# Optimization experiments

Hardware: AMD Instinct MI355X
Metric: run time of the kernel (lower is better)

The kernel has to match this reference:

```python
import jax, jax.numpy as jnp
import numpy as np

B, N, DIN, D, NH, NL = 4, 256, 4, 64, 4, 2
DH = D // NH
EPS = 1e-5
SLOPE = 0.01  # torch LeakyReLU default negative_slope


def setup_inputs() -> dict:
    key = jax.random.key(0)
    ks = jax.random.split(key, 16)
    def p(k, shape, s=0.05):
        return jax.random.normal(k, shape, jnp.float32) * s
    return {
        "feature": jax.random.normal(ks[0], (B, N, N, DIN), jnp.float32),
        "W1": p(ks[1], (DIN, D)), "b1": jnp.zeros((D,), jnp.float32),
        "mw": p(ks[2], (NH, D)), "mb": jnp.zeros((NH,), jnp.float32),
        "bn_gamma": jnp.ones((D,), jnp.float32), "bn_beta": jnp.zeros((D,), jnp.float32),
        "Wq": p(ks[3], (NL, D, D)), "bq": jnp.zeros((NL, D), jnp.float32),
        "Wk": p(ks[4], (NL, D, D)), "bk": jnp.zeros((NL, D), jnp.float32),
        "Wv": p(ks[5], (NL, D, D)), "bv": jnp.zeros((NL, D), jnp.float32),
        "Wo": p(ks[6], (NL, D, D)), "bo": jnp.zeros((NL, D), jnp.float32),
        "ln1_g": jnp.ones((NL, D), jnp.float32), "ln1_b": jnp.zeros((NL, D), jnp.float32),
        "Wff1": p(ks[7], (NL, D, 2 * D)), "bff1": jnp.zeros((NL, 2 * D), jnp.float32),
        "Wff2": p(ks[8], (NL, 2 * D, D)), "bff2": jnp.zeros((NL, D), jnp.float32),
        "ln2_g": jnp.ones((NL, D), jnp.float32), "ln2_b": jnp.zeros((NL, D), jnp.float32),
    }


def _leaky(x):
    return jnp.where(x >= 0, x, SLOPE * x)


def _layer_norm(x, g, b):
    m = x.mean(axis=-1, keepdims=True)
    v = x.var(axis=-1, keepdims=True)
    return g * (x - m) / jnp.sqrt(v + EPS) + b


def reference(feature, W1, b1, mw, mb, bn_gamma, bn_beta,
              Wq, bq, Wk, bk, Wv, bv, Wo, bo, ln1_g, ln1_b,
              Wff1, bff1, Wff2, bff2, ln2_g, ln2_b):
    # linear1: (B,N,N,DIN) -> (B,N,N,D)
    feat = feature @ W1 + b1
    # per-head scalar attention score over node pairs: (NH,B,N,N)
    s = jnp.einsum('bijh,nh->nbij', feat, mw) + mb[:, None, None, None]
    w = jnp.exp(_leaky(s))
    w = w / w.sum(axis=3, keepdims=True)  # softmax-like over second node dim j
    # weighted aggregation: sum over i, then mean over heads -> (B,N,D)
    h = jnp.einsum('nbij,bijh->bjh', w, feat) / NH
    # BatchNorm1d over channels D, stats over (B,N) (training-mode, biased var)
    m = h.mean(axis=(0, 1))
    v = h.var(axis=(0, 1))
    x = bn_gamma * (h - m) / jnp.sqrt(v + EPS) + bn_beta  # (B,N,D)
    # standard post-LN TransformerEncoder, NL layers
    scale = 1.0 / np.sqrt(DH).astype(np.float32)
    for l in range(NL):
        q = (x @ Wq[l] + bq[l]).reshape(B, N, NH, DH)
        k = (x @ Wk[l] + bk[l]).reshape(B, N, NH, DH)
        vv = (x @ Wv[l] + bv[l]).reshape(B, N, NH, DH)
        a = jax.nn.softmax(jnp.einsum('bqhd,bkhd->bhqk', q, k) * scale, axis=-1)
        o = jnp.einsum('bhqk,bkhd->bqhd', a, vv).reshape(B, N, D) @ Wo[l] + bo[l]
        x = _layer_norm(x + o, ln1_g[l], ln1_b[l])
        f = jax.nn.relu(x @ Wff1[l] + bff1[l]) @ Wff2[l] + bff2[l]
        x = _layer_norm(x + f, ln2_g[l], ln2_b[l])
    return x
```

## Files before the change

kernel.cpp:

```cpp
#include <hip/hip_runtime.h>
#include <math.h>

#define B 4
#define N 256
#define DIN 4
#define D 64
#define NH 4
#define NL 2
#define DH 16

constexpr float EPS = 1e-5f;
constexpr float SLOPE = 0.01f;

__global__ void __launch_bounds__(256) k_rowsum(
    const float* __restrict__ feature, const float* __restrict__ W1,
    const float* __restrict__ b1, const float* __restrict__ mw,
    const float* __restrict__ mb, float* __restrict__ rs,
    float* __restrict__ bnacc ) {
    __shared__ float M[16];
    __shared__ float C[4];
    int t = threadIdx.x;
    int lane = t & 63, w = t >> 6;
    int cb = blockIdx.x;
    if (cb == 0 && t < 128) bnacc[t] = 0.f;
    if (t < 16) {
        int n = t >> 2, kk = t & 3;
        float s = 0.f;
        for (int d = 0; d < D; ++d) s += W1[kk * D + d] * mw[n * D + d];
        M[t] = s;
    } else if (t < 20) {
        int n = t - 16;
        float s = mb[n];
        for (int d = 0; d < D; ++d) s += b1[d] * mw[n * D + d];
        C[n] = s;
    }
    __syncthreads();

    int bi = cb * 4 + w;
    const float4* fb = (const float4*)(feature) + (size_t)bi * N;
    float sn[4] = {0.f, 0.f, 0.f, 0.f};
#pragma unroll
    for (int m = 0; m < 4; ++m) {
        float4 f = fb[lane + 64 * m];
#pragma unroll
        for (int n = 0; n < 4; ++n) {
            float s = C[n] + f.x * M[n*4+0] + f.y * M[n*4+1] + f.z * M[n*4+2] + f.w * M[n*4+3];
            s = (s >= 0.f) ? s : SLOPE * s;
            sn[n] += __expf(s);
        }
    }
#pragma unroll
    for (int n = 0; n < 4; ++n)
#pragma unroll
        for (int off = 32; off > 0; off >>= 1) sn[n] += __shfl_xor(sn[n], off);
    if (lane == 0) {
        float4 o = {sn[0], sn[1], sn[2], sn[3]};
        *(float4*)(rs + (size_t)bi * 4) = o;
    }
}

__global__ void __launch_bounds__(256) k_aggregate(
    const float* __restrict__ feature, const float* __restrict__ W1,
    const float* __restrict__ b1, const float* __restrict__ mw,
    const float* __restrict__ mb, const float* __restrict__ rs,
    float* __restrict__ h, float* __restrict__ bnacc) {
    __shared__ float M[16];
    __shared__ float C[4];
    __shared__ float part[80];
    __shared__ float gacc[20];
    __shared__ float hs[4][D];
    int t = threadIdx.x;
    int lane = t & 63, w = t >> 6;
    int cb = blockIdx.x;
    if (t < 16) {
        int n = t >> 2, kk = t & 3;
        float s = 0.f;
        for (int d = 0; d < D; ++d) s += W1[kk * D + d] * mw[n * D + d];
        M[t] = s;
    } else if (t < 20) {
        int n = t - 16;
        float s = mb[n];
        for (int d = 0; d < D; ++d) s += b1[d] * mw[n * D + d];
        C[n] = s;
    }
    __syncthreads();

    int b = cb >> 6, j0 = (cb & 63) * 4;
    int i = t;
    const float4* fb = (const float4*)(feature) + ((size_t)(b * N + i) * N + j0);
    float4 f[4];
#pragma unroll
    for (int jj = 0; jj < 4; ++jj) f[jj] = fb[jj];
    float4 r4 = *(const float4*)(rs + (size_t)(b * N + i) * 4);
    float rinv[4] = {1.f / r4.x, 1.f / r4.y, 1.f / r4.z, 1.f / r4.w};
    float acc[4][5];
#pragma unroll
    for (int jj = 0; jj < 4; ++jj) {
        float wbar = 0.f;
#pragma unroll
        for (int n = 0; n < 4; ++n) {
            float s = C[n] + f[jj].x * M[n*4+0] + f[jj].y * M[n*4+1] + f[jj].z * M[n*4+2] + f[jj].w * M[n*4+3];
            s = (s >= 0.f) ? s : SLOPE * s;
            wbar += __expf(s) * rinv[n];
        }
        wbar *= 0.25f;
        acc[jj][0] = wbar * f[jj].x; acc[jj][1] = wbar * f[jj].y;
        acc[jj][2] = wbar * f[jj].z; acc[jj][3] = wbar * f[jj].w;
        acc[jj][4] = wbar;
    }
#pragma unroll
    for (int jj = 0; jj < 4; ++jj)
#pragma unroll
        for (int c = 0; c < 5; ++c)
#pragma unroll
            for (int off = 32; off > 0; off >>= 1) acc[jj][c] += __shfl_xor(acc[jj][c], off);
    if (lane == 0) {
#pragma unroll
        for (int jj = 0; jj < 4; ++jj)
#pragma unroll
            for (int c = 0; c < 5; ++c) part[w * 20 + jj * 5 + c] = acc[jj][c];
    }
    __syncthreads();
    if (t < 20) gacc[t] = part[t] + part[20 + t] + part[40 + t] + part[60 + t];
    __syncthreads();
    float hv = gacc[w * 5 + 4] * b1[lane];
#pragma unroll
    for (int kk = 0; kk < 4; ++kk) hv += gacc[w * 5 + kk] * W1[kk * D + lane];
    h[((size_t)(b * N + j0 + w)) * D + lane] = hv;
    hs[w][lane] = hv;
    __syncthreads();
    if (w == 0) {
        float s = hs[0][lane] + hs[1][lane] + hs[2][lane] + hs[3][lane];
        float sq = hs[0][lane]*hs[0][lane] + hs[1][lane]*hs[1][lane]
                 + hs[2][lane]*hs[2][lane] + hs[3][lane]*hs[3][lane];
        atomicAdd(bnacc + lane, s);
        atomicAdd(bnacc + D + lane, sq);
    }
}

__global__ void __launch_bounds__(256) k_qkv0(
    const float* __restrict__ h, const float* __restrict__ bnacc,
    const float* __restrict__ bn_g, const float* __restrict__ bn_b,
    const float* __restrict__ Wq, const float* __restrict__ bq,
    const float* __restrict__ Wk, const float* __restrict__ bk,
    const float* __restrict__ Wv, const float* __restrict__ bv,
    float* __restrict__ x, float* __restrict__ q,
    float* __restrict__ k, float* __restrict__ v) {
    __shared__ float xs[4][D];
    int t = threadIdx.x;
    int lane = t & 63, w = t >> 6;
    int token = blockIdx.x * 4 + w;
    int b = token >> 8, n = token & (N - 1);
    float mean = bnacc[lane] * (1.0f / (B * N));
    float var = bnacc[D + lane] * (1.0f / (B * N)) - mean * mean;
    float inv = rsqrtf(var + EPS);
    size_t xi = (size_t)token * D + lane;
    float xv = bn_g[lane] * (h[xi] - mean) * inv + bn_b[lane];
    x[xi] = xv;
    xs[w][lane] = xv;
    __syncthreads();
    int head = lane >> 4, dh = lane & (DH - 1);
    size_t oidx = (((size_t)(b * NH + head)) * N + n) * DH + dh;
    float aq = bq[lane], ak = bk[lane], av = bv[lane];
#pragma unroll 8
    for (int kk = 0; kk < D; ++kk) {
        float s0 = xs[w][kk];
        aq += s0 * Wq[kk * D + lane];
        ak += s0 * Wk[kk * D + lane];
        av += s0 * Wv[kk * D + lane];
    }
    q[oidx] = aq; k[oidx] = ak; v[oidx] = av;
}

__global__ void __launch_bounds__(256, 2) k_layer(
    const float* __restrict__ q, const float* __restrict__ k,
    const float* __restrict__ v,
    const float* __restrict__ Wo, const float* __restrict__ bo,
    const float* __restrict__ ln1g, const float* __restrict__ ln1b,
    const float* __restrict__ Wff1, const float* __restrict__ bff1,
    const float* __restrict__ Wff2, const float* __restrict__ bff2,
    const float* __restrict__ ln2g, const float* __restrict__ ln2b,
    const float* __restrict__ Wqn, const float* __restrict__ bqn,
    const float* __restrict__ Wkn, const float* __restrict__ bkn,
    const float* __restrict__ Wvn, const float* __restrict__ bvn,
    float* __restrict__ qo, float* __restrict__ ko, float* __restrict__ vo,
    float* __restrict__ x) {
    __shared__ float attS[4][D];
    __shared__ float xs1[4][D];
    __shared__ float f1s[4][2 * D];
    int t = threadIdx.x;
    int lane = t & 63, w = t >> 6;
    int b = blockIdx.x;
    int q0 = blockIdx.y * 4;
    int bh = b * NH + w;

    const float* kb = k + (size_t)bh * N * DH;
    const float* vb = v + (size_t)bh * N * DH;
    float4 Kr[4][4], Vr[4][4];
#pragma unroll
    for (int j = 0; j < 4; ++j) {
        int key = lane + 64 * j;
#pragma unroll
        for (int c = 0; c < 4; ++c) {
            Kr[j][c] = *(const float4*)(kb + (size_t)key * DH + 4 * c);
            Vr[j][c] = *(const float4*)(vb + (size_t)key * DH + 4 * c);
        }
    }
#pragma unroll
    for (int qq = 0; qq < 4; ++qq) {
        const float* qp = q + ((size_t)bh * N + q0 + qq) * DH;
        float sq[DH];
#pragma unroll
        for (int d = 0; d < DH; ++d) sq[d] = qp[d] * 0.25f;
        float s[4];
#pragma unroll
        for (int j = 0; j < 4; ++j) {
            float a = 0.f;
#pragma unroll
            for (int c = 0; c < 4; ++c)
                a += sq[4*c+0]*Kr[j][c].x + sq[4*c+1]*Kr[j][c].y +
                     sq[4*c+2]*Kr[j][c].z + sq[4*c+3]*Kr[j][c].w;
            s[j] = a;
        }
        float m = fmaxf(fmaxf(s[0], s[1]), fmaxf(s[2], s[3]));
#pragma unroll
        for (int off = 32; off > 0; off >>= 1) m = fmaxf(m, __shfl_xor(m, off));
        float p[4], lsum = 0.f;
#pragma unroll
        for (int j = 0; j < 4; ++j) { p[j] = __expf(s[j] - m); lsum += p[j]; }
#pragma unroll
        for (int off = 32; off > 0; off >>= 1) lsum += __shfl_xor(lsum, off);
        float o[DH];
#pragma unroll
        for (int d = 0; d < DH; ++d) o[d] = 0.f;
#pragma unroll
        for (int j = 0; j < 4; ++j) {
#pragma unroll
            for (int c = 0; c < 4; ++c) {
                o[4*c+0] += p[j] * Vr[j][c].x;
                o[4*c+1] += p[j] * Vr[j][c].y;
                o[4*c+2] += p[j] * Vr[j][c].z;
                o[4*c+3] += p[j] * Vr[j][c].w;
            }
        }
#pragma unroll
        for (int d = 0; d < DH; ++d) {
#pragma unroll
            for (int off = 32; off > 0; off >>= 1) o[d] += __shfl_xor(o[d], off);
        }
        if (lane == 0) {
            float rl = 1.f / lsum;
#pragma unroll
            for (int d = 0; d < DH; ++d) attS[qq][w * DH + d] = o[d] * rl;
        }
    }
    __syncthreads();

    int token = q0 + w;
    int ch = lane;
    size_t xidx = ((size_t)b * N + token) * D + ch;
    float oo = bo[ch];
#pragma unroll 8
    for (int kk = 0; kk < D; ++kk) oo += attS[w][kk] * Wo[kk * D + ch];
    float r = x[xidx] + oo;
    float s1 = r, sq1 = r * r;
#pragma unroll
    for (int off = 32; off > 0; off >>= 1) {
        s1 += __shfl_xor(s1, off);
        sq1 += __shfl_xor(sq1, off);
    }
    float mean1 = s1 * (1.0f / D);
    float var1 = sq1 * (1.0f / D) - mean1 * mean1;
    float x1 = ln1g[ch] * (r - mean1) * rsqrtf(var1 + EPS) + ln1b[ch];
    xs1[w][ch] = x1;
    __syncthreads();

    float a0 = bff1[ch], a1 = bff1[ch + 64];
#pragma unroll 8
    for (int kk = 0; kk < D; ++kk) {
        float xv = xs1[w][kk];
        a0 += xv * Wff1[kk * 2 * D + ch];
        a1 += xv * Wff1[kk * 2 * D + ch + 64];
    }
    f1s[w][ch] = fmaxf(a0, 0.f);
    f1s[w][ch + 64] = fmaxf(a1, 0.f);
    __syncthreads();

    float o2 = bff2[ch];
#pragma unroll 8
    for (int kk = 0; kk < 2 * D; ++kk) o2 += f1s[w][kk] * Wff2[kk * D + ch];
    float r2 = x1 + o2;
    float s2 = r2, sq2 = r2 * r2;
#pragma unroll
    for (int off = 32; off > 0; off >>= 1) {
        s2 += __shfl_xor(s2, off);
        sq2 += __shfl_xor(sq2, off);
    }
    float mean2 = s2 * (1.0f / D);
    float var2 = sq2 * (1.0f / D) - mean2 * mean2;
    float xnew = ln2g[ch] * (r2 - mean2) * rsqrtf(var2 + EPS) + ln2b[ch];
    x[xidx] = xnew;

    if (Wqn != nullptr) {
        __syncthreads();
        attS[w][ch] = xnew;
        __syncthreads();
        int head = ch >> 4, dh = ch & (DH - 1);
        size_t oidx = (((size_t)(b * NH + head)) * N + token) * DH + dh;
        float aq = bqn[ch], ak = bkn[ch], av = bvn[ch];
#pragma unroll 8
        for (int kk = 0; kk < D; ++kk) {
            float s0 = attS[w][kk];
            aq += s0 * Wqn[kk * D + ch];
            ak += s0 * Wkn[kk * D + ch];
            av += s0 * Wvn[kk * D + ch];
        }
        qo[oidx] = aq; ko[oidx] = ak; vo[oidx] = av;
    }
}

extern "C" void kernel_launch(void* const* d_in, const int* in_sizes, int n_in,
                              void* d_out, int out_size, void* d_ws, size_t ws_size,
                              hipStream_t stream) {
    const float* feature = (const float*)d_in[0];
    const float* W1   = (const float*)d_in[1];
    const float* b1   = (const float*)d_in[2];
    const float* mw   = (const float*)d_in[3];
    const float* mb   = (const float*)d_in[4];
    const float* bn_g = (const float*)d_in[5];
    const float* bn_b = (const float*)d_in[6];
    const float* Wq   = (const float*)d_in[7];
    const float* bq   = (const float*)d_in[8];
    const float* Wk   = (const float*)d_in[9];
    const float* bk   = (const float*)d_in[10];
    const float* Wv   = (const float*)d_in[11];
    const float* bv   = (const float*)d_in[12];
    const float* Wo   = (const float*)d_in[13];
    const float* bo   = (const float*)d_in[14];
    const float* ln1g = (const float*)d_in[15];
    const float* ln1b = (const float*)d_in[16];
    const float* Wff1 = (const float*)d_in[17];
    const float* bff1 = (const float*)d_in[18];
    const float* Wff2 = (const float*)d_in[19];
    const float* bff2 = (const float*)d_in[20];
    const float* ln2g = (const float*)d_in[21];
    const float* ln2b = (const float*)d_in[22];

    float* ws    = (float*)d_ws;
    float* rs    = ws;
    float* h     = rs + B * N * NH;
    float* bnacc = h + B * N * D;
    float* q     = bnacc + 128;
    float* k     = q + B * N * D;
    float* v     = k + B * N * D;
    float* x     = (float*)d_out;

    k_rowsum<<<256, 256, 0, stream>>>(feature, W1, b1, mw, mb, rs, bnacc);
    k_aggregate<<<256, 256, 0, stream>>>(feature, W1, b1, mw, mb, rs, h, bnacc);
    k_qkv0<<<256, 256, 0, stream>>>(h, bnacc, bn_g, bn_b,
                                    Wq, bq, Wk, bk, Wv, bv, x, q, k, v);
    k_layer<<<dim3(B, N / 4), 256, 0, stream>>>(q, k, v,
        Wo, bo, ln1g, ln1b, Wff1, bff1, Wff2, bff2, ln2g, ln2b,
        Wq + (size_t)D * D, bq + D, Wk + (size_t)D * D, bk + D,
        Wv + (size_t)D * D, bv + D, q, k, v, x);
    k_layer<<<dim3(B, N / 4), 256, 0, stream>>>(q, k, v,
        Wo + (size_t)D * D, bo + D, ln1g + D, ln1b + D,
        Wff1 + (size_t)D * 2 * D, bff1 + 2 * D,
        Wff2 + (size_t)2 * D * D, bff2 + D, ln2g + D, ln2b + D,
        nullptr, nullptr, nullptr, nullptr, nullptr, nullptr,
        nullptr, nullptr, nullptr, x);
}
```

Before: 164.1 us.

## Stage weights into LDS asynchronously and split-K matvecs across 512-thread blocks

```diff
diff --git a/kernel.cpp b/kernel.cpp
--- a/kernel.cpp
+++ b/kernel.cpp
@@ -11,6 +11,19 @@
 
 constexpr float EPS = 1e-5f;
 constexpr float SLOPE = 0.01f;
+
+template <int NF4>
+__device__ __forceinline__ void stage(float* dst, const float* src, int t) {
+    int lane = t & 63, w = t >> 6;
+#pragma unroll
+    for (int i0 = 0; i0 < NF4; i0 += 512) {
+        int base = i0 + w * 64;
+        __builtin_amdgcn_global_load_lds(
+            (const __attribute__((address_space(1))) void*)(src + 4 * (base + lane)),
+            (__attribute__((address_space(3))) void*)(dst + 4 * base),
+            16, 0, 0);
+    }
+}
 
 __global__ void __launch_bounds__(256) k_rowsum(
     const float* __restrict__ feature, const float* __restrict__ W1,
@@ -138,7 +151,7 @@
     }
 }
 
-__global__ void __launch_bounds__(256) k_qkv0(
+__global__ void __launch_bounds__(512, 2) k_qkv0(
     const float* __restrict__ h, const float* __restrict__ bnacc,
     const float* __restrict__ bn_g, const float* __restrict__ bn_b,
     const float* __restrict__ Wq, const float* __restrict__ bq,
@@ -146,33 +159,62 @@
     const float* __restrict__ Wv, const float* __restrict__ bv,
     float* __restrict__ x, float* __restrict__ q,
     float* __restrict__ k, float* __restrict__ v) {
-    __shared__ float xs[4][D];
+    __shared__ __align__(16) float xsh[4 * D];
+    __shared__ __align__(16) float pp[8 * 192];
+    __shared__ __align__(16) float WqL[D * D];
+    __shared__ __align__(16) float WkL[D * D];
+    __shared__ __align__(16) float WvL[D * D];
     int t = threadIdx.x;
     int lane = t & 63, w = t >> 6;
-    int token = blockIdx.x * 4 + w;
+    int tok4 = w & 3, kh = w >> 2;
+    int token = blockIdx.x * 4 + tok4;
     int b = token >> 8, n = token & (N - 1);
-    float mean = bnacc[lane] * (1.0f / (B * N));
-    float var = bnacc[D + lane] * (1.0f / (B * N)) - mean * mean;
+    int ch = lane;
+
+    stage<D * D / 4>(WqL, Wq, t);
+    stage<D * D / 4>(WkL, Wk, t);
+    stage<D * D / 4>(WvL, Wv, t);
+
+    float mean = bnacc[ch] * (1.0f / (B * N));
+    float var = bnacc[D + ch] * (1.0f / (B * N)) - mean * mean;
     float inv = rsqrtf(var + EPS);
-    size_t xi = (size_t)token * D + lane;
-    float xv = bn_g[lane] * (h[xi] - mean) * inv + bn_b[lane];
-    x[xi] = xv;
-    xs[w][lane] = xv;
-    __syncthreads();
-    int head = lane >> 4, dh = lane & (DH - 1);
-    size_t oidx = (((size_t)(b * NH + head)) * N + n) * DH + dh;
-    float aq = bq[lane], ak = bk[lane], av = bv[lane];
-#pragma unroll 8
-    for (int kk = 0; kk < D; ++kk) {
-        float s0 = xs[w][kk];
-        aq += s0 * Wq[kk * D + lane];
-        ak += s0 * Wk[kk * D + lane];
-        av += s0 * Wv[kk * D + lane];
-    }
-    q[oidx] = aq; k[oidx] = ak; v[oidx] = av;
-}
-
-__global__ void __launch_bounds__(256, 2) k_layer(
+    size_t xi = (size_t)token * D + ch;
+    float xv = bn_g[ch] * (h[xi] - mean) * inv + bn_b[ch];
+    float bq_r = bq[ch], bk_r = bk[ch], bv_r = bv[ch];
+    if (kh == 0) {
+        x[xi] = xv;
+        xsh[tok4 * D + ch] = xv;
+    }
+    __syncthreads();
+
+    const float4* xr4 = (const float4*)(xsh + tok4 * D + kh * 32);
+    float aq0=0.f, aq1=0.f, ak0=0.f, ak1=0.f, av0=0.f, av1=0.f;
+#pragma unroll
+    for (int k4 = 0; k4 < 8; ++k4) {
+        float4 xx = xr4[k4];
+        int kk = kh * 32 + k4 * 4;
+        aq0 += xx.x * WqL[(kk+0)*D+ch] + xx.z * WqL[(kk+2)*D+ch];
+        aq1 += xx.y * WqL[(kk+1)*D+ch] + xx.w * WqL[(kk+3)*D+ch];
+        ak0 += xx.x * WkL[(kk+0)*D+ch] + xx.z * WkL[(kk+2)*D+ch];
+        ak1 += xx.y * WkL[(kk+1)*D+ch] + xx.w * WkL[(kk+3)*D+ch];
+        av0 += xx.x * WvL[(kk+0)*D+ch] + xx.z * WvL[(kk+2)*D+ch];
+        av1 += xx.y * WvL[(kk+1)*D+ch] + xx.w * WvL[(kk+3)*D+ch];
+    }
+    float* ppw = pp + w * 192;
+    ppw[ch] = aq0 + aq1;
+    ppw[64 + ch] = ak0 + ak1;
+    ppw[128 + ch] = av0 + av1;
+    __syncthreads();
+    if (kh == 0) {
+        int head = ch >> 4, dh = ch & (DH - 1);
+        size_t oidx = (((size_t)(b * NH + head)) * N + n) * DH + dh;
+        q[oidx] = bq_r + pp[tok4*192 + ch] + pp[(tok4+4)*192 + ch];
+        k[oidx] = bk_r + pp[tok4*192 + 64 + ch] + pp[(tok4+4)*192 + 64 + ch];
+        v[oidx] = bv_r + pp[tok4*192 + 128 + ch] + pp[(tok4+4)*192 + 128 + ch];
+    }
+}
+
+__global__ void __launch_bounds__(512, 2) k_layer(
     const float* __restrict__ q, const float* __restrict__ k,
     const float* __restrict__ v,
     const float* __restrict__ Wo, const float* __restrict__ bo,
@@ -185,15 +227,27 @@
     const float* __restrict__ Wvn, const float* __restrict__ bvn,
     float* __restrict__ qo, float* __restrict__ ko, float* __restrict__ vo,
     float* __restrict__ x) {
-    __shared__ float attS[4][D];
-    __shared__ float xs1[4][D];
-    __shared__ float f1s[4][2 * D];
+    __shared__ __align__(16) float attS[4 * D];
+    __shared__ __align__(16) float xs1[4 * D];
+    __shared__ __align__(16) float f1s[4 * 2 * D];
+    __shared__ __align__(16) float pp[8 * 192];
+    __shared__ __align__(16) float WoL[D * D];
+    __shared__ __align__(16) float Wff1L[D * 2 * D];
+    __shared__ __align__(16) float Wff2L[2 * D * D];
+    __shared__ __align__(16) float WqnL[D * D];
+    __shared__ __align__(16) float WknL[D * D];
+    __shared__ __align__(16) float WvnL[D * D];
+
     int t = threadIdx.x;
     int lane = t & 63, w = t >> 6;
     int b = blockIdx.x;
     int q0 = blockIdx.y * 4;
-    int bh = b * NH + w;
-
+    int h_ = w & 3, qpair = w >> 2;
+    int tok4 = w & 3, kh = w >> 2;
+    int token = q0 + tok4;
+    int ch = lane;
+
+    int bh = b * NH + h_;
     const float* kb = k + (size_t)bh * N * DH;
     const float* vb = v + (size_t)bh * N * DH;
     float4 Kr[4][4], Vr[4][4];
@@ -206,12 +260,31 @@
             Vr[j][c] = *(const float4*)(vb + (size_t)key * DH + 4 * c);
         }
     }
-#pragma unroll
-    for (int qq = 0; qq < 4; ++qq) {
+
+    size_t xidx = ((size_t)b * N + token) * D + ch;
+    float xv = x[xidx];
+    float bo_r = bo[ch], l1g = ln1g[ch], l1b = ln1b[ch];
+    float bf1_r = bff1[kh * D + ch];
+    float bf2_r = bff2[ch], l2g = ln2g[ch], l2b = ln2b[ch];
+    float bq_r = 0.f, bk_r = 0.f, bv_r = 0.f;
+    if (Wqn != nullptr) { bq_r = bqn[ch]; bk_r = bkn[ch]; bv_r = bvn[ch]; }
+
+    stage<1024>(WoL, Wo, t);
+    stage<2048>(Wff1L, Wff1, t);
+    stage<2048>(Wff2L, Wff2, t);
+    if (Wqn != nullptr) {
+        stage<1024>(WqnL, Wqn, t);
+        stage<1024>(WknL, Wkn, t);
+        stage<1024>(WvnL, Wvn, t);
+    }
+
+#pragma unroll
+    for (int qq2 = 0; qq2 < 2; ++qq2) {
+        int qq = qpair * 2 + qq2;
         const float* qp = q + ((size_t)bh * N + q0 + qq) * DH;
         float sq[DH];
 #pragma unroll
-        for (int d = 0; d < DH; ++d) sq[d] = qp[d] * 0.25f;
+        for (int d = 0; d < DH; ++d) sq[d] = qp[d];
         float s[4];
 #pragma unroll
         for (int j = 0; j < 4; ++j) {
@@ -227,7 +300,7 @@
         for (int off = 32; off > 0; off >>= 1) m = fmaxf(m, __shfl_xor(m, off));
         float p[4], lsum = 0.f;
 #pragma unroll
-        for (int j = 0; j < 4; ++j) { p[j] = __expf(s[j] - m); lsum += p[j]; }
+        for (int j = 0; j < 4; ++j) { p[j] = __expf((s[j] - m) * 0.25f); lsum += p[j]; }
 #pragma unroll
         for (int off = 32; off > 0; off >>= 1) lsum += __shfl_xor(lsum, off);
         float o[DH];
@@ -251,18 +324,29 @@
         if (lane == 0) {
             float rl = 1.f / lsum;
 #pragma unroll
-            for (int d = 0; d < DH; ++d) attS[qq][w * DH + d] = o[d] * rl;
-        }
-    }
-    __syncthreads();
-
-    int token = q0 + w;
-    int ch = lane;
-    size_t xidx = ((size_t)b * N + token) * D + ch;
-    float oo = bo[ch];
-#pragma unroll 8
-    for (int kk = 0; kk < D; ++kk) oo += attS[w][kk] * Wo[kk * D + ch];
-    float r = x[xidx] + oo;
+            for (int d = 0; d < DH; ++d) attS[qq * D + h_ * DH + d] = o[d] * rl;
+        }
+    }
+    __syncthreads();
+
+    float* ppw = pp + w * 192;
+    {
+        const float4* ar4 = (const float4*)(attS + tok4 * D + kh * 32);
+        float a0=0.f, a1=0.f, a2=0.f, a3=0.f;
+#pragma unroll
+        for (int k4 = 0; k4 < 8; ++k4) {
+            float4 av = ar4[k4];
+            int kk = kh * 32 + k4 * 4;
+            a0 += av.x * WoL[(kk+0)*D+ch];
+            a1 += av.y * WoL[(kk+1)*D+ch];
+            a2 += av.z * WoL[(kk+2)*D+ch];
+            a3 += av.w * WoL[(kk+3)*D+ch];
+        }
+        ppw[ch] = (a0+a1)+(a2+a3);
+    }
+    __syncthreads();
+    float oo = bo_r + pp[tok4*192 + ch] + pp[(tok4+4)*192 + ch];
+    float r = xv + oo;
     float s1 = r, sq1 = r * r;
 #pragma unroll
     for (int off = 32; off > 0; off >>= 1) {
@@ -271,24 +355,50 @@
     }
     float mean1 = s1 * (1.0f / D);
     float var1 = sq1 * (1.0f / D) - mean1 * mean1;
-    float x1 = ln1g[ch] * (r - mean1) * rsqrtf(var1 + EPS) + ln1b[ch];
-    xs1[w][ch] = x1;
-    __syncthreads();
-
-    float a0 = bff1[ch], a1 = bff1[ch + 64];
-#pragma unroll 8
-    for (int kk = 0; kk < D; ++kk) {
-        float xv = xs1[w][kk];
-        a0 += xv * Wff1[kk * 2 * D + ch];
-        a1 += xv * Wff1[kk * 2 * D + ch + 64];
-    }
-    f1s[w][ch] = fmaxf(a0, 0.f);
-    f1s[w][ch + 64] = fmaxf(a1, 0.f);
-    __syncthreads();
-
-    float o2 = bff2[ch];
-#pragma unroll 8
-    for (int kk = 0; kk < 2 * D; ++kk) o2 += f1s[w][kk] * Wff2[kk * D + ch];
+    float x1 = l1g * (r - mean1) * rsqrtf(var1 + EPS) + l1b;
+    if (kh == 0) xs1[tok4 * D + ch] = x1;
+    __syncthreads();
+
+    {
+        const float4* xr4 = (const float4*)(xs1 + tok4 * D + kh * 32);
+        float u0=0.f,u1=0.f,u2=0.f,u3=0.f, g0=0.f,g1=0.f,g2=0.f,g3=0.f;
+#pragma unroll
+        for (int k4 = 0; k4 < 8; ++k4) {
+            float4 xx = xr4[k4];
+            int kk = kh * 32 + k4 * 4;
+            u0 += xx.x * Wff1L[(kk+0)*128+ch];
+            u1 += xx.y * Wff1L[(kk+1)*128+ch];
+            u2 += xx.z * Wff1L[(kk+2)*128+ch];
+            u3 += xx.w * Wff1L[(kk+3)*128+ch];
+            g0 += xx.x * Wff1L[(kk+0)*128+64+ch];
+            g1 += xx.y * Wff1L[(kk+1)*128+64+ch];
+            g2 += xx.z * Wff1L[(kk+2)*128+64+ch];
+            g3 += xx.w * Wff1L[(kk+3)*128+64+ch];
+        }
+        ppw[ch] = (u0+u1)+(u2+u3);
+        ppw[64+ch] = (g0+g1)+(g2+g3);
+    }
+    __syncthreads();
+    f1s[tok4*128 + kh*64 + ch] =
+        fmaxf(pp[tok4*192 + kh*64 + ch] + pp[(tok4+4)*192 + kh*64 + ch] + bf1_r, 0.f);
+    __syncthreads();
+
+    {
+        const float4* fr4 = (const float4*)(f1s + tok4*128 + kh*64);
+        float e0=0.f,e1=0.f,e2=0.f,e3=0.f;
+#pragma unroll
+        for (int k4 = 0; k4 < 16; ++k4) {
+            float4 fv = fr4[k4];
+            int kk = kh*64 + k4*4;
+            e0 += fv.x * Wff2L[(kk+0)*D+ch];
+            e1 += fv.y * Wff2L[(kk+1)*D+ch];
+            e2 += fv.z * Wff2L[(kk+2)*D+ch];
+            e3 += fv.w * Wff2L[(kk+3)*D+ch];
+        }
+        ppw[ch] = (e0+e1)+(e2+e3);
+    }
+    __syncthreads();
+    float o2 = bf2_r + pp[tok4*192 + ch] + pp[(tok4+4)*192 + ch];
     float r2 = x1 + o2;
     float s2 = r2, sq2 = r2 * r2;
 #pragma unroll
@@ -298,24 +408,36 @@
     }
     float mean2 = s2 * (1.0f / D);
     float var2 = sq2 * (1.0f / D) - mean2 * mean2;
-    float xnew = ln2g[ch] * (r2 - mean2) * rsqrtf(var2 + EPS) + ln2b[ch];
-    x[xidx] = xnew;
+    float xnew = l2g * (r2 - mean2) * rsqrtf(var2 + EPS) + l2b;
+    if (kh == 0) x[xidx] = xnew;
 
     if (Wqn != nullptr) {
+        if (kh == 0) attS[tok4 * D + ch] = xnew;
         __syncthreads();
-        attS[w][ch] = xnew;
+        const float4* xr4 = (const float4*)(attS + tok4 * D + kh * 32);
+        float aq0=0.f, aq1=0.f, ak0=0.f, ak1=0.f, av0=0.f, av1=0.f;
+#pragma unroll
+        for (int k4 = 0; k4 < 8; ++k4) {
+            float4 xx = xr4[k4];
+            int kk = kh * 32 + k4 * 4;
+            aq0 += xx.x * WqnL[(kk+0)*D+ch] + xx.z * WqnL[(kk+2)*D+ch];
+            aq1 += xx.y * WqnL[(kk+1)*D+ch] + xx.w * WqnL[(kk+3)*D+ch];
+            ak0 += xx.x * WknL[(kk+0)*D+ch] + xx.z * WknL[(kk+2)*D+ch];
+            ak1 += xx.y * WknL[(kk+1)*D+ch] + xx.w * WknL[(kk+3)*D+ch];
+            av0 += xx.x * WvnL[(kk+0)*D+ch] + xx.z * WvnL[(kk+2)*D+ch];
+            av1 += xx.y * WvnL[(kk+1)*D+ch] + xx.w * WvnL[(kk+3)*D+ch];
+        }
+        ppw[ch] = aq0 + aq1;
+        ppw[64+ch] = ak0 + ak1;
+        ppw[128+ch] = av0 + av1;
         __syncthreads();
-        int head = ch >> 4, dh = ch & (DH - 1);
-        size_t oidx = (((size_t)(b * NH + head)) * N + token) * DH + dh;
-        float aq = bqn[ch], ak = bkn[ch], av = bvn[ch];
-#pragma unroll 8
-        for (int kk = 0; kk < D; ++kk) {
-            float s0 = attS[w][kk];
-            aq += s0 * Wqn[kk * D + ch];
-            ak += s0 * Wkn[kk * D + ch];
-            av += s0 * Wvn[kk * D + ch];
-        }
-        qo[oidx] = aq; ko[oidx] = ak; vo[oidx] = av;
+        if (kh == 0) {
+            int head = ch >> 4, dh = ch & (DH - 1);
+            size_t oidx = (((size_t)(b * NH + head)) * N + token) * DH + dh;
+            qo[oidx] = bq_r + pp[tok4*192 + ch] + pp[(tok4+4)*192 + ch];
+            ko[oidx] = bk_r + pp[tok4*192 + 64 + ch] + pp[(tok4+4)*192 + 64 + ch];
+            vo[oidx] = bv_r + pp[tok4*192 + 128 + ch] + pp[(tok4+4)*192 + 128 + ch];
+        }
     }
 }
 
@@ -357,13 +479,13 @@
 
     k_rowsum<<<256, 256, 0, stream>>>(feature, W1, b1, mw, mb, rs, bnacc);
     k_aggregate<<<256, 256, 0, stream>>>(feature, W1, b1, mw, mb, rs, h, bnacc);
-    k_qkv0<<<256, 256, 0, stream>>>(h, bnacc, bn_g, bn_b,
+    k_qkv0<<<256, 512, 0, stream>>>(h, bnacc, bn_g, bn_b,
                                     Wq, bq, Wk, bk, Wv, bv, x, q, k, v);
-    k_layer<<<dim3(B, N / 4), 256, 0, stream>>>(q, k, v,
+    k_layer<<<dim3(B, N / 4), 512, 0, stream>>>(q, k, v,
         Wo, bo, ln1g, ln1b, Wff1, bff1, Wff2, bff2, ln2g, ln2b,
         Wq + (size_t)D * D, bq + D, Wk + (size_t)D * D, bk + D,
         Wv + (size_t)D * D, bv + D, q, k, v, x);
-    k_layer<<<dim3(B, N / 4), 256, 0, stream>>>(q, k, v,
+    k_layer<<<dim3(B, N / 4), 512, 0, stream>>>(q, k, v,
         Wo + (size_t)D * D, bo + D, ln1g + D, ln1b + D,
         Wff1 + (size_t)D * 2 * D, bff1 + 2 * D,
         Wff2 + (size_t)2 * D * D, bff2 + D, ln2g + D, ln2b + D,
```

Result: faster. 147.8 us (-10.0%).

## Split per-token work across waves with split-K reductions and one token per block

Applied to the files above, without the earlier changes.

```diff
diff --git a/kernel.cpp b/kernel.cpp
--- a/kernel.cpp
+++ b/kernel.cpp
@@ -12,13 +12,14 @@
 constexpr float EPS = 1e-5f;
 constexpr float SLOPE = 0.01f;
 
-__global__ void __launch_bounds__(256) k_rowsum(
+__global__ void __launch_bounds__(512) k_rowsum(
     const float* __restrict__ feature, const float* __restrict__ W1,
     const float* __restrict__ b1, const float* __restrict__ mw,
     const float* __restrict__ mb, float* __restrict__ rs,
     float* __restrict__ bnacc ) {
     __shared__ float M[16];
     __shared__ float C[4];
+    __shared__ float part[32];
     int t = threadIdx.x;
     int lane = t & 63, w = t >> 6;
     int cb = blockIdx.x;
@@ -36,12 +37,13 @@
     }
     __syncthreads();
 
-    int bi = cb * 4 + w;
+    int r = w & 3, mh = w >> 2;
+    int bi = cb * 4 + r;
     const float4* fb = (const float4*)(feature) + (size_t)bi * N;
     float sn[4] = {0.f, 0.f, 0.f, 0.f};
 #pragma unroll
-    for (int m = 0; m < 4; ++m) {
-        float4 f = fb[lane + 64 * m];
+    for (int mm = 0; mm < 2; ++mm) {
+        float4 f = fb[lane + 64 * (mh * 2 + mm)];
 #pragma unroll
         for (int n = 0; n < 4; ++n) {
             float s = C[n] + f.x * M[n*4+0] + f.y * M[n*4+1] + f.z * M[n*4+2] + f.w * M[n*4+3];
@@ -54,19 +56,24 @@
 #pragma unroll
         for (int off = 32; off > 0; off >>= 1) sn[n] += __shfl_xor(sn[n], off);
     if (lane == 0) {
-        float4 o = {sn[0], sn[1], sn[2], sn[3]};
-        *(float4*)(rs + (size_t)bi * 4) = o;
+#pragma unroll
+        for (int n = 0; n < 4; ++n) part[w * 4 + n] = sn[n];
+    }
+    __syncthreads();
+    if (t < 16) {
+        int rr = t >> 2, n = t & 3;
+        rs[((size_t)(cb * 4 + rr)) * 4 + n] = part[rr * 4 + n] + part[(rr + 4) * 4 + n];
     }
 }
 
-__global__ void __launch_bounds__(256) k_aggregate(
+__global__ void __launch_bounds__(512) k_aggregate(
     const float* __restrict__ feature, const float* __restrict__ W1,
     const float* __restrict__ b1, const float* __restrict__ mw,
     const float* __restrict__ mb, const float* __restrict__ rs,
     float* __restrict__ h, float* __restrict__ bnacc) {
     __shared__ float M[16];
     __shared__ float C[4];
-    __shared__ float part[80];
+    __shared__ float part[8][10];
     __shared__ float gacc[20];
     __shared__ float hs[4][D];
     int t = threadIdx.x;
@@ -86,16 +93,16 @@
     __syncthreads();
 
     int b = cb >> 6, j0 = (cb & 63) * 4;
-    int i = t;
-    const float4* fb = (const float4*)(feature) + ((size_t)(b * N + i) * N + j0);
-    float4 f[4];
-#pragma unroll
-    for (int jj = 0; jj < 4; ++jj) f[jj] = fb[jj];
+    int i = t & 255, jh = t >> 8;
+    const float4* fb = (const float4*)(feature) + ((size_t)(b * N + i) * N + j0 + jh * 2);
+    float4 f[2];
+    f[0] = fb[0];
+    f[1] = fb[1];
     float4 r4 = *(const float4*)(rs + (size_t)(b * N + i) * 4);
     float rinv[4] = {1.f / r4.x, 1.f / r4.y, 1.f / r4.z, 1.f / r4.w};
-    float acc[4][5];
-#pragma unroll
-    for (int jj = 0; jj < 4; ++jj) {
+    float acc[2][5];
+#pragma unroll
+    for (int jj = 0; jj < 2; ++jj) {
         float wbar = 0.f;
 #pragma unroll
         for (int n = 0; n < 4; ++n) {
@@ -109,27 +116,34 @@
         acc[jj][4] = wbar;
     }
 #pragma unroll
-    for (int jj = 0; jj < 4; ++jj)
+    for (int jj = 0; jj < 2; ++jj)
 #pragma unroll
         for (int c = 0; c < 5; ++c)
 #pragma unroll
             for (int off = 32; off > 0; off >>= 1) acc[jj][c] += __shfl_xor(acc[jj][c], off);
     if (lane == 0) {
 #pragma unroll
-        for (int jj = 0; jj < 4; ++jj)
-#pragma unroll
-            for (int c = 0; c < 5; ++c) part[w * 20 + jj * 5 + c] = acc[jj][c];
-    }
-    __syncthreads();
-    if (t < 20) gacc[t] = part[t] + part[20 + t] + part[40 + t] + part[60 + t];
-    __syncthreads();
-    float hv = gacc[w * 5 + 4] * b1[lane];
-#pragma unroll
-    for (int kk = 0; kk < 4; ++kk) hv += gacc[w * 5 + kk] * W1[kk * D + lane];
-    h[((size_t)(b * N + j0 + w)) * D + lane] = hv;
-    hs[w][lane] = hv;
-    __syncthreads();
-    if (w == 0) {
+        for (int jj = 0; jj < 2; ++jj)
+#pragma unroll
+            for (int c = 0; c < 5; ++c) part[w][jj * 5 + c] = acc[jj][c];
+    }
+    __syncthreads();
+    if (t < 20) {
+        int jj = t / 5, c = t - jj * 5;
+        int g = jj >> 1, jjl = jj & 1;
+        gacc[t] = part[g*4+0][jjl*5+c] + part[g*4+1][jjl*5+c]
+                + part[g*4+2][jjl*5+c] + part[g*4+3][jjl*5+c];
+    }
+    __syncthreads();
+    if (t < 256) {
+        float hv = gacc[w * 5 + 4] * b1[lane];
+#pragma unroll
+        for (int kk = 0; kk < 4; ++kk) hv += gacc[w * 5 + kk] * W1[kk * D + lane];
+        h[((size_t)(b * N + j0 + w)) * D + lane] = hv;
+        hs[w][lane] = hv;
+    }
+    __syncthreads();
+    if (t < 64) {
         float s = hs[0][lane] + hs[1][lane] + hs[2][lane] + hs[3][lane];
         float sq = hs[0][lane]*hs[0][lane] + hs[1][lane]*hs[1][lane]
                  + hs[2][lane]*hs[2][lane] + hs[3][lane]*hs[3][lane];
@@ -138,7 +152,7 @@
     }
 }
 
-__global__ void __launch_bounds__(256) k_qkv0(
+__global__ void __launch_bounds__(256, 4) k_qkv0(
     const float* __restrict__ h, const float* __restrict__ bnacc,
     const float* __restrict__ bn_g, const float* __restrict__ bn_b,
     const float* __restrict__ Wq, const float* __restrict__ bq,
@@ -146,33 +160,38 @@
     const float* __restrict__ Wv, const float* __restrict__ bv,
     float* __restrict__ x, float* __restrict__ q,
     float* __restrict__ k, float* __restrict__ v) {
-    __shared__ float xs[4][D];
-    int t = threadIdx.x;
-    int lane = t & 63, w = t >> 6;
-    int token = blockIdx.x * 4 + w;
-    int b = token >> 8, n = token & (N - 1);
-    float mean = bnacc[lane] * (1.0f / (B * N));
-    float var = bnacc[D + lane] * (1.0f / (B * N)) - mean * mean;
+    __shared__ float pp[4][192];
+    int t = threadIdx.x, lane = t & 63, w = t >> 6, ch = lane;
+    int b = blockIdx.x, n = blockIdx.y;
+    int token = b * N + n;
+    float mean = bnacc[ch] * (1.0f / (B * N));
+    float var = bnacc[D + ch] * (1.0f / (B * N)) - mean * mean;
     float inv = rsqrtf(var + EPS);
-    size_t xi = (size_t)token * D + lane;
-    float xv = bn_g[lane] * (h[xi] - mean) * inv + bn_b[lane];
-    x[xi] = xv;
-    xs[w][lane] = xv;
-    __syncthreads();
-    int head = lane >> 4, dh = lane & (DH - 1);
-    size_t oidx = (((size_t)(b * NH + head)) * N + n) * DH + dh;
-    float aq = bq[lane], ak = bk[lane], av = bv[lane];
-#pragma unroll 8
-    for (int kk = 0; kk < D; ++kk) {
-        float s0 = xs[w][kk];
-        aq += s0 * Wq[kk * D + lane];
-        ak += s0 * Wk[kk * D + lane];
-        av += s0 * Wv[kk * D + lane];
-    }
-    q[oidx] = aq; k[oidx] = ak; v[oidx] = av;
+    float xv = bn_g[ch] * (h[(size_t)token * D + ch] - mean) * inv + bn_b[ch];
+    if (w == 0) x[(size_t)token * D + ch] = xv;
+    float aq = 0.f, ak = 0.f, av = 0.f;
+#pragma unroll
+    for (int i = 0; i < 16; ++i) {
+        int kk = w * 16 + i;
+        float xx = __shfl(xv, kk);
+        aq += xx * Wq[kk * D + ch];
+        ak += xx * Wk[kk * D + ch];
+        av += xx * Wv[kk * D + ch];
+    }
+    pp[w][ch] = aq; pp[w][64 + ch] = ak; pp[w][128 + ch] = av;
+    __syncthreads();
+    if (w < 3) {
+        int o = w * 64;
+        float val = pp[0][o + ch] + pp[1][o + ch] + pp[2][o + ch] + pp[3][o + ch];
+        int head = ch >> 4, dh = ch & (DH - 1);
+        size_t oidx = (((size_t)(b * NH + head)) * N + n) * DH + dh;
+        if (w == 0) q[oidx] = val + bq[ch];
+        else if (w == 1) k[oidx] = val + bk[ch];
+        else v[oidx] = val + bv[ch];
+    }
 }
 
-__global__ void __launch_bounds__(256, 2) k_layer(
+__global__ void __launch_bounds__(256, 4) k_layer(
     const float* __restrict__ q, const float* __restrict__ k,
     const float* __restrict__ v,
     const float* __restrict__ Wo, const float* __restrict__ bo,
@@ -185,84 +204,76 @@
     const float* __restrict__ Wvn, const float* __restrict__ bvn,
     float* __restrict__ qo, float* __restrict__ ko, float* __restrict__ vo,
     float* __restrict__ x) {
-    __shared__ float attS[4][D];
-    __shared__ float xs1[4][D];
-    __shared__ float f1s[4][2 * D];
-    int t = threadIdx.x;
-    int lane = t & 63, w = t >> 6;
-    int b = blockIdx.x;
-    int q0 = blockIdx.y * 4;
+    __shared__ float attS[D];
+    __shared__ float ppA[4][192];
+    __shared__ float ppB[4][192];
+    int t = threadIdx.x, lane = t & 63, w = t >> 6, ch = lane;
+    int b = blockIdx.x, n = blockIdx.y;
+    int token = b * N + n;
+    size_t xidx = (size_t)token * D + ch;
+    float xv = x[xidx];
+
     int bh = b * NH + w;
-
+    const float* qp = q + ((size_t)bh * N + n) * DH;
+    float4 qv[4];
+#pragma unroll
+    for (int c = 0; c < 4; ++c) qv[c] = ((const float4*)qp)[c];
     const float* kb = k + (size_t)bh * N * DH;
     const float* vb = v + (size_t)bh * N * DH;
-    float4 Kr[4][4], Vr[4][4];
-#pragma unroll
-    for (int j = 0; j < 4; ++j) {
-        int key = lane + 64 * j;
+    float o[DH];
+#pragma unroll
+    for (int d = 0; d < DH; ++d) o[d] = 0.f;
+    float l = 0.f;
+#pragma unroll 2
+    for (int cc = 0; cc < 4; ++cc) {
+        int key = cc * 64 + lane;
+        const float4* kp4 = (const float4*)(kb + (size_t)key * DH);
+        const float4* vp4 = (const float4*)(vb + (size_t)key * DH);
+        float4 Kc[4], Vc[4];
+#pragma unroll
+        for (int c = 0; c < 4; ++c) { Kc[c] = kp4[c]; Vc[c] = vp4[c]; }
+        float s = 0.f;
+#pragma unroll
+        for (int c = 0; c < 4; ++c)
+            s += qv[c].x * Kc[c].x + qv[c].y * Kc[c].y +
+                 qv[c].z * Kc[c].z + qv[c].w * Kc[c].w;
+        float p = __expf(s * 0.25f);
+        l += p;
 #pragma unroll
         for (int c = 0; c < 4; ++c) {
-            Kr[j][c] = *(const float4*)(kb + (size_t)key * DH + 4 * c);
-            Vr[j][c] = *(const float4*)(vb + (size_t)key * DH + 4 * c);
-        }
-    }
-#pragma unroll
-    for (int qq = 0; qq < 4; ++qq) {
-        const float* qp = q + ((size_t)bh * N + q0 + qq) * DH;
-        float sq[DH];
-#pragma unroll
-        for (int d = 0; d < DH; ++d) sq[d] = qp[d] * 0.25f;
-        float s[4];
-#pragma unroll
-        for (int j = 0; j < 4; ++j) {
-            float a = 0.f;
-#pragma unroll
-            for (int c = 0; c < 4; ++c)
-                a += sq[4*c+0]*Kr[j][c].x + sq[4*c+1]*Kr[j][c].y +
-                     sq[4*c+2]*Kr[j][c].z + sq[4*c+3]*Kr[j][c].w;
-            s[j] = a;
-        }
-        float m = fmaxf(fmaxf(s[0], s[1]), fmaxf(s[2], s[3]));
-#pragma unroll
-        for (int off = 32; off > 0; off >>= 1) m = fmaxf(m, __shfl_xor(m, off));
-        float p[4], lsum = 0.f;
-#pragma unroll
-        for (int j = 0; j < 4; ++j) { p[j] = __expf(s[j] - m); lsum += p[j]; }
-#pragma unroll
-        for (int off = 32; off > 0; off >>= 1) lsum += __shfl_xor(lsum, off);
-        float o[DH];
-#pragma unroll
-        for (int d = 0; d < DH; ++d) o[d] = 0.f;
-#pragma unroll
-        for (int j = 0; j < 4; ++j) {
-#pragma unroll
-            for (int c = 0; c < 4; ++c) {
-                o[4*c+0] += p[j] * Vr[j][c].x;
-                o[4*c+1] += p[j] * Vr[j][c].y;
-                o[4*c+2] += p[j] * Vr[j][c].z;
-                o[4*c+3] += p[j] * Vr[j][c].w;
-            }
-        }
-#pragma unroll
-        for (int d = 0; d < DH; ++d) {
-#pragma unroll
-            for (int off = 32; off > 0; off >>= 1) o[d] += __shfl_xor(o[d], off);
-        }
-        if (lane == 0) {
-            float rl = 1.f / lsum;
-#pragma unroll
-            for (int d = 0; d < DH; ++d) attS[qq][w * DH + d] = o[d] * rl;
-        }
-    }
-    __syncthreads();
-
-    int token = q0 + w;
-    int ch = lane;
-    size_t xidx = ((size_t)b * N + token) * D + ch;
-    float oo = bo[ch];
-#pragma unroll 8
-    for (int kk = 0; kk < D; ++kk) oo += attS[w][kk] * Wo[kk * D + ch];
-    float r = x[xidx] + oo;
+            o[4*c+0] += p * Vc[c].x;
+            o[4*c+1] += p * Vc[c].y;
+            o[4*c+2] += p * Vc[c].z;
+            o[4*c+3] += p * Vc[c].w;
+        }
+    }
+#pragma unroll
+    for (int off = 32; off > 0; off >>= 1) l += __shfl_xor(l, off);
+#pragma unroll
+    for (int d = 0; d < DH; ++d)
+#pragma unroll
+        for (int off = 32; off > 0; off >>= 1) o[d] += __shfl_xor(o[d], off);
+    float rl = 1.f / l;
+    if (lane < DH) {
+        float sel = o[0];
+#pragma unroll
+        for (int d = 1; d < DH; ++d) if (lane == d) sel = o[d];
+        attS[w * DH + lane] = sel * rl;
+    }
+    __syncthreads();
+
+    {
+        float acc = 0.f;
+#pragma unroll
+        for (int i = 0; i < 16; ++i) {
+            int kk = w * 16 + i;
+            acc += attS[kk] * Wo[kk * D + ch];
+        }
+        ppA[w][ch] = acc;
+    }
+    __syncthreads();
+    float oo = bo[ch] + ppA[0][ch] + ppA[1][ch] + ppA[2][ch] + ppA[3][ch];
+    float r = xv + oo;
     float s1 = r, sq1 = r * r;
 #pragma unroll
     for (int off = 32; off > 0; off >>= 1) {
@@ -272,23 +283,36 @@
     float mean1 = s1 * (1.0f / D);
     float var1 = sq1 * (1.0f / D) - mean1 * mean1;
     float x1 = ln1g[ch] * (r - mean1) * rsqrtf(var1 + EPS) + ln1b[ch];
-    xs1[w][ch] = x1;
-    __syncthreads();
-
-    float a0 = bff1[ch], a1 = bff1[ch + 64];
-#pragma unroll 8
-    for (int kk = 0; kk < D; ++kk) {
-        float xv = xs1[w][kk];
-        a0 += xv * Wff1[kk * 2 * D + ch];
-        a1 += xv * Wff1[kk * 2 * D + ch + 64];
-    }
-    f1s[w][ch] = fmaxf(a0, 0.f);
-    f1s[w][ch + 64] = fmaxf(a1, 0.f);
-    __syncthreads();
-
-    float o2 = bff2[ch];
-#pragma unroll 8
-    for (int kk = 0; kk < 2 * D; ++kk) o2 += f1s[w][kk] * Wff2[kk * D + ch];
+
+    {
+        float u = 0.f, g = 0.f;
+#pragma unroll
+        for (int i = 0; i < 16; ++i) {
+            int kk = w * 16 + i;
+            float xx = __shfl(x1, kk);
+            u += xx * Wff1[kk * 2 * D + ch];
+            g += xx * Wff1[kk * 2 * D + D + ch];
+        }
+        ppB[w][ch] = u; ppB[w][64 + ch] = g;
+    }
+    __syncthreads();
+    float f1lo = fmaxf(bff1[ch] + ppB[0][ch] + ppB[1][ch] + ppB[2][ch] + ppB[3][ch], 0.f);
+    float f1hi = fmaxf(bff1[D + ch] + ppB[0][64+ch] + ppB[1][64+ch] + ppB[2][64+ch] + ppB[3][64+ch], 0.f);
+
+    {
+        float src = (w < 2) ? f1lo : f1hi;
+        int kb0 = (w & 1) * 32;
+        float acc = 0.f;
+#pragma unroll
+        for (int i = 0; i < 32; ++i) {
+            int kk = (w >> 1) * 64 + kb0 + i;
+            float xx = __shfl(src, kb0 + i);
+            acc += xx * Wff2[kk * D + ch];
+        }
+        ppA[w][ch] = acc;
+    }
+    __syncthreads();
+    float o2 = bff2[ch] + ppA[0][ch] + ppA[1][ch] + ppA[2][ch] + ppA[3][ch];
     float r2 = x1 + o2;
     float s2 = r2, sq2 = r2 * r2;
 #pragma unroll
@@ -299,23 +323,29 @@
     float mean2 = s2 * (1.0f / D);
     float var2 = sq2 * (1.0f / D) - mean2 * mean2;
     float xnew = ln2g[ch] * (r2 - mean2) * rsqrtf(var2 + EPS) + ln2b[ch];
-    x[xidx] = xnew;
+    if (w == 0) x[xidx] = xnew;
 
     if (Wqn != nullptr) {
+        float aq = 0.f, ak = 0.f, avv = 0.f;
+#pragma unroll
+        for (int i = 0; i < 16; ++i) {
+            int kk = w * 16 + i;
+            float xx = __shfl(xnew, kk);
+            aq  += xx * Wqn[kk * D + ch];
+            ak  += xx * Wkn[kk * D + ch];
+            avv += xx * Wvn[kk * D + ch];
+        }
+        ppB[w][ch] = aq; ppB[w][64 + ch] = ak; ppB[w][128 + ch] = avv;
         __syncthreads();
-        attS[w][ch] = xnew;
-        __syncthreads();
-        int head = ch >> 4, dh = ch & (DH - 1);
-        size_t oidx = (((size_t)(b * NH + head)) * N + token) * DH + dh;
-        float aq = bqn[ch], ak = bkn[ch], av = bvn[ch];
-#pragma unroll 8
-        for (int kk = 0; kk < D; ++kk) {
-            float s0 = attS[w][kk];
-            aq += s0 * Wqn[kk * D + ch];
-            ak += s0 * Wkn[kk * D + ch];
-            av += s0 * Wvn[kk * D + ch];
-        }
-        qo[oidx] = aq; ko[oidx] = ak; vo[oidx] = av;
+        if (w < 3) {
+            int off = w * 64;
+            float val = ppB[0][off+ch] + ppB[1][off+ch] + ppB[2][off+ch] + ppB[3][off+ch];
+            int head = ch >> 4, dh = ch & (DH - 1);
+            size_t oidx = (((size_t)(b * NH + head)) * N + n) * DH + dh;
+            if (w == 0) qo[oidx] = val + bqn[ch];
+            else if (w == 1) ko[oidx] = val + bkn[ch];
+            else vo[oidx] = val + bvn[ch];
+        }
     }
 }
 
@@ -348,22 +378,24 @@
 
     float* ws    = (float*)d_ws;
     float* rs    = ws;
-    float* h     = rs + B * N * NH;
-    float* bnacc = h + B * N * D;
-    float* q     = bnacc + 128;
-    float* k     = q + B * N * D;
-    float* v     = k + B * N * D;
+    float* bnacc = rs + B * N * NH;
+    float* h     = bnacc + 128;
+    float* q     = h + B * N * D;
+    float* k0    = q + B * N * D;
+    float* v0    = k0 + B * N * D;
+    float* k1    = v0 + B * N * D;
+    float* v1    = k1 + B * N * D;
     float* x     = (float*)d_out;
 
-    k_rowsum<<<256, 256, 0, stream>>>(feature, W1, b1, mw, mb, rs, bnacc);
-    k_aggregate<<<256, 256, 0, stream>>>(feature, W1, b1, mw, mb, rs, h, bnacc);
-    k_qkv0<<<256, 256, 0, stream>>>(h, bnacc, bn_g, bn_b,
-                                    Wq, bq, Wk, bk, Wv, bv, x, q, k, v);
-    k_layer<<<dim3(B, N / 4), 256, 0, stream>>>(q, k, v,
+    k_rowsum<<<256, 512, 0, stream>>>(feature, W1, b1, mw, mb, rs, bnacc);
+    k_aggregate<<<256, 512, 0, stream>>>(feature, W1, b1, mw, mb, rs, h, bnacc);
+    k_qkv0<<<dim3(B, N), 256, 0, stream>>>(h, bnacc, bn_g, bn_b,
+                                           Wq, bq, Wk, bk, Wv, bv, x, q, k0, v0);
+    k_layer<<<dim3(B, N), 256, 0, stream>>>(q, k0, v0,
         Wo, bo, ln1g, ln1b, Wff1, bff1, Wff2, bff2, ln2g, ln2b,
         Wq + (size_t)D * D, bq + D, Wk + (size_t)D * D, bk + D,
-        Wv + (size_t)D * D, bv + D, q, k, v, x);
-    k_layer<<<dim3(B, N / 4), 256, 0, stream>>>(q, k, v,
+        Wv + (size_t)D * D, bv + D, q, k1, v1, x);
+    k_layer<<<dim3(B, N), 256, 0, stream>>>(q, k1, v1,
         Wo + (size_t)D * D, bo + D, ln1g + D, ln1b + D,
         Wff1 + (size_t)D * 2 * D, bff1 + 2 * D,
         Wff2 + (size_t)2 * D * D, bff2 + D, ln2g + D, ln2b + D,
```

New measurement: 153.0 us. -6.8%, faster.
